# Performance work log

Hardware: AMD Instinct MI355X
Metric: run time of the kernel (lower is better)

Reference implementation:

```python
import jax, jax.numpy as jnp
import numpy as np

PATCH_SIZE = 16  # init_kwargs patch_size


def setup_inputs() -> dict:
    key = jax.random.key(0)
    k1, k2, k3 = jax.random.split(key, 3)
    B, C, H, W = 128, 3, 224, 224
    n_points = int(H * W * 0.5 / PATCH_SIZE ** 2)  # 98
    imgs = jax.random.normal(k1, (B, C, H, W), dtype=jnp.float32)
    points_x = jax.random.randint(k2, (B, n_points), 0, H - PATCH_SIZE + 1, dtype=jnp.int32)
    points_y = jax.random.randint(k3, (B, n_points), 0, W - PATCH_SIZE + 1, dtype=jnp.int32)
    return {"imgs": imgs, "points_x": points_x, "points_y": points_y}


def reference(imgs, points_x, points_y):
    # imgs: [B, C, H, W]; points_x/points_y: [B, N] top-left corners of P x P patches to zero.
    B, C, H, W = imgs.shape
    P = PATCH_SIZE
    off = jnp.arange(P, dtype=points_x.dtype)
    b = jnp.arange(B)[:, None, None, None]                       # [B,1,1,1]
    xs = points_x[:, :, None, None] + off[None, None, :, None]    # [B,N,P,1]
    ys = points_y[:, :, None, None] + off[None, None, None, :]    # [B,N,1,P]
    # Build occlusion mask once with a single scatter, then apply across channels.
    mask = jnp.zeros((B, H, W), dtype=jnp.bool_).at[b, xs, ys].set(True)  # [B,H,W]
    return jnp.where(mask[:, None, :, :], jnp.zeros((), imgs.dtype), imgs)
```

## Files before the change

kernel.cpp:

```cpp
#include <hip/hip_runtime.h>

#define BB 128
#define CC 3
#define HH 224
#define WW 224
#define PP 16

#define W4 (WW / 4)
#define PER_IMG4 (CC * HH * W4)
#define NWORDS (HH * 7)
#define TOTAL4 (BB * PER_IMG4)

typedef float vfloat4 __attribute__((ext_vector_type(4)));

__global__ __launch_bounds__(256) void occl_build(
        unsigned int* __restrict__ gmask,
        const int* __restrict__ px, const int* __restrict__ py, int N) {
    __shared__ unsigned int rowbits[NWORDS];
    const int t = threadIdx.x;
    const int b = blockIdx.x;

    for (int i = t; i < NWORDS; i += 256) rowbits[i] = 0u;
    __syncthreads();

    const int nrow = N * PP;
    for (int r = t; r < nrow; r += 256) {
        int p = r >> 4;
        int i = r & (PP - 1);
        int x = px[b * N + p] + i;
        int y = py[b * N + p];
        unsigned long long mm = 0xFFFFull << (y & 31);
        int w0 = x * 7 + (y >> 5);
        atomicOr(&rowbits[w0], (unsigned int)mm);
        unsigned int hi = (unsigned int)(mm >> 32);
        if (hi) atomicOr(&rowbits[w0 + 1], hi);
    }
    __syncthreads();

    unsigned int* dst = gmask + (size_t)b * NWORDS;
    for (int i = t; i < NWORDS; i += 256) dst[i] = rowbits[i];
}

__global__ __launch_bounds__(256) void occl_apply(
        vfloat4* __restrict__ out, const vfloat4* __restrict__ imgs,
        const unsigned int* __restrict__ gmask) {
    int f = blockIdx.x * 256 + threadIdx.x;
    int w4 = f % W4;
    int t  = f / W4;
    int h  = t % HH;
    int b  = t / (HH * CC);
    unsigned int word = gmask[(size_t)b * NWORDS + h * 7 + (w4 >> 3)];
    unsigned int m4 = (word >> ((w4 & 7) * 4)) & 0xFu;
    vfloat4 v = imgs[f];
    if (m4 & 1u) v.x = 0.f;
    if (m4 & 2u) v.y = 0.f;
    if (m4 & 4u) v.z = 0.f;
    if (m4 & 8u) v.w = 0.f;
    __builtin_nontemporal_store(v, &out[f]);
}

extern "C" void kernel_launch(void* const* d_in, const int* in_sizes, int n_in,
                              void* d_out, int out_size, void* d_ws, size_t ws_size,
                              hipStream_t stream) {
    const float* imgs = (const float*)d_in[0];
    const int*   px   = (const int*)d_in[1];
    const int*   py   = (const int*)d_in[2];
    float*       out  = (float*)d_out;

    const int N = in_sizes[1] / BB;

    occl_build<<<BB, 256, 0, stream>>>((unsigned int*)d_ws, px, py, N);
    occl_apply<<<TOTAL4 / 256, 256, 0, stream>>>(
        (vfloat4*)out, (const vfloat4*)imgs, (const unsigned int*)d_ws);
}
```

Before: 139.3 us.

## Fuse mask build into apply kernel with per-block local row mask

Removes the separate mask-building kernel and its global mask buffer. Each apply block now builds a small shared-memory bitmask covering only the few image rows its 256 float4 elements touch, scanning all patch points and OR-ing bits for rows that overlap. The image load is issued before the barrier to hide its latency. In exchange, every block re-reads the point arrays and does redundant per-point work, and the code assumes N is at most 256 and that a block spans at most 6 rows within a single channel.

```diff
diff --git a/kernel.cpp b/kernel.cpp
--- a/kernel.cpp
+++ b/kernel.cpp
@@ -7,51 +7,56 @@
 #define PP 16
 
 #define W4 (WW / 4)
-#define PER_IMG4 (CC * HH * W4)
-#define NWORDS (HH * 7)
+#define CHAN4 (HH * W4)
+#define PER_IMG4 (CC * CHAN4)
 #define TOTAL4 (BB * PER_IMG4)
+#define NROWS 6
 
 typedef float vfloat4 __attribute__((ext_vector_type(4)));
 
-__global__ __launch_bounds__(256) void occl_build(
-        unsigned int* __restrict__ gmask,
+__global__ __launch_bounds__(256) void occl_fused(
+        vfloat4* __restrict__ out, const vfloat4* __restrict__ imgs,
         const int* __restrict__ px, const int* __restrict__ py, int N) {
-    __shared__ unsigned int rowbits[NWORDS];
     const int t = threadIdx.x;
-    const int b = blockIdx.x;
+    const int blockF0 = blockIdx.x * 256;
+    const int f = blockF0 + t;
 
-    for (int i = t; i < NWORDS; i += 256) rowbits[i] = 0u;
+    const int b       = blockF0 / PER_IMG4;
+    const int localF0 = blockF0 % CHAN4;
+    const int h0      = localF0 / W4;
+
+    __shared__ unsigned int rowbits[NROWS * 7];
+
+    if (t < NROWS * 7) rowbits[t] = 0u;
+
+    vfloat4 v = imgs[f];
+
     __syncthreads();
 
-    const int nrow = N * PP;
-    for (int r = t; r < nrow; r += 256) {
-        int p = r >> 4;
-        int i = r & (PP - 1);
-        int x = px[b * N + p] + i;
-        int y = py[b * N + p];
-        unsigned long long mm = 0xFFFFull << (y & 31);
-        int w0 = x * 7 + (y >> 5);
-        atomicOr(&rowbits[w0], (unsigned int)mm);
-        unsigned int hi = (unsigned int)(mm >> 32);
-        if (hi) atomicOr(&rowbits[w0 + 1], hi);
+    if (t < N) {
+        int x = px[b * N + t];
+        int y = py[b * N + t];
+        int lo = x > h0 ? x : h0;
+        int hi = (x + PP < h0 + NROWS) ? (x + PP) : (h0 + NROWS);
+        if (lo < hi) {
+            unsigned long long mm = 0xFFFFull << (y & 31);
+            unsigned int lo32 = (unsigned int)mm;
+            unsigned int hi32 = (unsigned int)(mm >> 32);
+            int woff = y >> 5;
+            for (int h = lo; h < hi; ++h) {
+                int base = (h - h0) * 7 + woff;
+                atomicOr(&rowbits[base], lo32);
+                if (hi32) atomicOr(&rowbits[base + 1], hi32);
+            }
+        }
     }
     __syncthreads();
 
-    unsigned int* dst = gmask + (size_t)b * NWORDS;
-    for (int i = t; i < NWORDS; i += 256) dst[i] = rowbits[i];
-}
-
-__global__ __launch_bounds__(256) void occl_apply(
-        vfloat4* __restrict__ out, const vfloat4* __restrict__ imgs,
-        const unsigned int* __restrict__ gmask) {
-    int f = blockIdx.x * 256 + threadIdx.x;
-    int w4 = f % W4;
-    int t  = f / W4;
-    int h  = t % HH;
-    int b  = t / (HH * CC);
-    unsigned int word = gmask[(size_t)b * NWORDS + h * 7 + (w4 >> 3)];
+    int lf = localF0 + t;
+    int w4 = lf % W4;
+    int h  = lf / W4;
+    unsigned int word = rowbits[(h - h0) * 7 + (w4 >> 3)];
     unsigned int m4 = (word >> ((w4 & 7) * 4)) & 0xFu;
-    vfloat4 v = imgs[f];
     if (m4 & 1u) v.x = 0.f;
     if (m4 & 2u) v.y = 0.f;
     if (m4 & 4u) v.z = 0.f;
@@ -69,7 +74,6 @@
 
     const int N = in_sizes[1] / BB;
 
-    occl_build<<<BB, 256, 0, stream>>>((unsigned int*)d_ws, px, py, N);
-    occl_apply<<<TOTAL4 / 256, 256, 0, stream>>>(
-        (vfloat4*)out, (const vfloat4*)imgs, (const unsigned int*)d_ws);
+    occl_fused<<<TOTAL4 / 256, 256, 0, stream>>>(
+        (vfloat4*)out, (const vfloat4*)imgs, px, py, N);
 }
```

After: 137.7 us. About the same (-1.2%).
